# Performance work log

Hardware: AMD Instinct MI355X
Metric: run time of the kernel (lower is better)

## Reference

```python
import jax, jax.numpy as jnp
import numpy as np

WINDOW_SIZE = 128
LOOK_BACKWARD = 1
LOOK_FORWARD = 0  # causal
PAD_VALUE = -1


def look_around(x, backward=LOOK_BACKWARD, forward=LOOK_FORWARD, pad_value=PAD_VALUE):
    # x: [..., windows, window_size, ...]; pad along the windows axis (axis=1)
    # and concatenate shifted copies along the window_size axis (axis=2).
    w = x.shape[1]
    pad_width = [(0, 0), (backward, forward)] + [(0, 0)] * (x.ndim - 2)
    padded = jnp.pad(x, pad_width, constant_values=pad_value)
    return jnp.concatenate([padded[:, i:i + w] for i in range(forward + backward + 1)], axis=2)


def setup_inputs() -> dict:
    key = jax.random.key(0)
    kq, kk, kv = jax.random.split(key, 3)
    shape = (2, 16, 8192, 64)
    return {
        "q": jax.random.normal(kq, shape, dtype=jnp.float32),
        "k": jax.random.normal(kk, shape, dtype=jnp.float32),
        "v": jax.random.normal(kv, shape, dtype=jnp.float32),
    }


def reference(q, k, v):
    shape = q.shape
    t, e = shape[-2], shape[-1]
    ws = WINDOW_SIZE
    assert t % ws == 0
    windows = t // ws
    scale = e ** (-0.5)

    # merge batch and head dims
    bq, bk, bv = (x.reshape(-1, windows, ws, e) for x in (q, k, v))
    b = bq.shape[0]

    # position ticker, bucketed: [1, windows, ws]
    b_t = jnp.arange(t, dtype=jnp.int32).reshape(1, windows, ws)

    bk = look_around(bk)                      # [b, windows, 2*ws, e]
    bv = look_around(bv)
    bq_t = b_t                                # [1, windows, ws]
    bq_k = look_around(b_t)                   # [1, windows, 2*ws]

    # scores: [b, windows, ws, 2*ws]
    dots = jnp.einsum('bwie,bwje->bwij', bq, bk) * scale
    mask_value = -jnp.finfo(dots.dtype).max

    # causal mask: query position must be >= key position
    causal_mask = bq_t[..., :, None] < bq_k[..., None, :]
    # padding mask from look_around fill
    pad_mask = (bq_k == PAD_VALUE)[:, :, None, :]
    dots = jnp.where(causal_mask | pad_mask, mask_value, dots)

    attn = jax.nn.softmax(dots, axis=-1)
    out = jnp.einsum('bwij,bwje->bwie', attn, bv)  # [b, windows, ws, e]
    return out.reshape(shape)
```

## Files before the change

### kernel.cpp

```cpp
#include <hip/hip_runtime.h>
#include <stdint.h>

typedef float f32x16 __attribute__((ext_vector_type(16)));
typedef short bf16x8 __attribute__((ext_vector_type(8)));
typedef uint32_t u32;

#define T_LEN 8192
#define E_DIM 64
#define WSZ   128
#define NWIN  64
#define NBH   32
#define SCALE 0.125f

union Frag { u32 w[4]; bf16x8 v; };

__device__ __forceinline__ u32 pkbf(float a, float b) {
    u32 r;
    asm("v_cvt_pk_bf16_f32 %0, %1, %2" : "=v"(r) : "v"(a), "v"(b));
    return r;
}

__device__ __forceinline__ u32 kaddr(u32 key, u32 bir) {
    return (key * 128u + bir) ^ ((key & 15u) << 4);
}

__device__ __forceinline__ void pv_half(const f32x16& a, int ksbase, int h, int ql,
                                        long krow0, const float* __restrict__ vg,
                                        f32x16& o0, f32x16& o1) {
    u32 W[8];
#pragma unroll
    for (int j = 0; j < 8; ++j) W[j] = pkbf(a[2 * j], a[2 * j + 1]);
#pragma unroll
    for (int hi = 0; hi < 2; ++hi) {
        const u32 w0 = W[4 * hi + 0], w1 = W[4 * hi + 1];
        const u32 w2 = W[4 * hi + 2], w3 = W[4 * hi + 3];
        const u32 y0 = (u32)__shfl_xor((int)w0, 32);
        const u32 y1 = (u32)__shfl_xor((int)w1, 32);
        const u32 y2 = (u32)__shfl_xor((int)w2, 32);
        const u32 y3 = (u32)__shfl_xor((int)w3, 32);
        Frag au;
        au.w[0] = h ? y2 : w0;
        au.w[1] = h ? y3 : w1;
        au.w[2] = h ? w2 : y0;
        au.w[3] = h ? w3 : y1;
        const int ks = ksbase + hi;
        const long vr = (krow0 + (long)(16 * ks + 8 * h)) * E_DIM + ql;
        float v0[8], v1[8];
#pragma unroll
        for (int j = 0; j < 8; ++j) {
            v0[j] = vg[vr + (long)j * E_DIM];
            v1[j] = vg[vr + (long)j * E_DIM + 32];
        }
        Frag b0, b1;
#pragma unroll
        for (int j = 0; j < 4; ++j) {
            b0.w[j] = pkbf(v0[2 * j], v0[2 * j + 1]);
            b1.w[j] = pkbf(v1[2 * j], v1[2 * j + 1]);
        }
        o0 = __builtin_amdgcn_mfma_f32_32x32x16_bf16(au.v, b0.v, o0, 0, 0, 0);
        o1 = __builtin_amdgcn_mfma_f32_32x32x16_bf16(au.v, b1.v, o1, 0, 0, 0);
    }
}

__global__ __launch_bounds__(256, 3)
void lattn_kernel(const float* __restrict__ qg, const float* __restrict__ kg,
                  const float* __restrict__ vg, float* __restrict__ outg) {
    __shared__ __align__(16) char lds[32768];

    const int tid  = threadIdx.x;
    const int lane = tid & 63;
    const int wid  = tid >> 6;
    const int h    = lane >> 5;
    const int ql   = lane & 31;

    const int bid = blockIdx.x;
    const int swz = ((bid & 7) << 8) | (bid >> 3);
    const int bh  = swz >> 6;
    const int w   = swz & 63;

    const size_t qrow0 = (size_t)bh * T_LEN + (size_t)w * WSZ;
    const long   krow0 = (long)bh * T_LEN + (long)(w - 1) * WSZ;

    Frag qf[4];
    {
        const float* qp = qg + (qrow0 + (size_t)(wid * 32 + ql)) * E_DIM;
#pragma unroll
        for (int ks = 0; ks < 4; ++ks) {
            float4 a = *(const float4*)(qp + ks * 16 + h * 8);
            float4 b = *(const float4*)(qp + ks * 16 + h * 8 + 4);
            qf[ks].w[0] = pkbf(a.x * SCALE, a.y * SCALE);
            qf[ks].w[1] = pkbf(a.z * SCALE, a.w * SCALE);
            qf[ks].w[2] = pkbf(b.x * SCALE, b.y * SCALE);
            qf[ks].w[3] = pkbf(b.z * SCALE, b.w * SCALE);
        }
    }

#pragma unroll
    for (int i = 0; i < 16; ++i) {
        const int f   = i * 256 + tid;
        const int row = f >> 4;
        const int c   = f & 15;
        if (w > 0 || row >= 128) {
            const float4 kv = *(const float4*)(kg + (size_t)(krow0 + row) * E_DIM + c * 4);
            *(uint2*)(lds + kaddr((u32)row, (u32)c * 8u)) =
                make_uint2(pkbf(kv.x, kv.y), pkbf(kv.z, kv.w));
        }
    }
    __syncthreads();

    const int qpos = wid * 32 + ql;
    f32x16 o0, o1;
#pragma unroll
    for (int r = 0; r < 16; ++r) { o0[r] = 0.f; o1[r] = 0.f; }
    float den = 0.f;

    const int qp0 = (w == 0) ? 2 : 0;
    for (int qp = qp0; qp < 4; ++qp) {
#pragma unroll
        for (int kf2 = 0; kf2 < 2; ++kf2) {
            f32x16 a;
#pragma unroll
            for (int r = 0; r < 16; ++r) a[r] = 0.f;
#pragma unroll
            for (int ks = 0; ks < 4; ++ks) {
                const bf16x8 kf = *(const bf16x8*)(lds +
                    kaddr((u32)(64 * qp + 32 * kf2 + ql), (u32)(32 * ks + 16 * h)));
                a = __builtin_amdgcn_mfma_f32_32x32x16_bf16(kf, qf[ks].v, a, 0, 0, 0);
            }
            const int kb = 64 * qp + 32 * kf2 + 4 * h - 128;
#pragma unroll
            for (int r = 0; r < 16; ++r) {
                const int kr = kb + (r & 3) + 8 * (r >> 2);
                float p = __expf(a[r]);
                p = (kr <= qpos) ? p : 0.f;
                a[r] = p;
                den += p;
            }
            pv_half(a, 4 * qp + 2 * kf2, h, ql, krow0, vg, o0, o1);
        }
    }

    den += __shfl_xor(den, 32);
    const float invd = 1.f / den;

    float* ob = outg + (qrow0 + (size_t)(wid * 32)) * E_DIM;
#pragma unroll
    for (int r = 0; r < 16; ++r) {
        const int rowq = (r & 3) + 8 * (r >> 2) + 4 * h;
        const float dn = __shfl(invd, rowq);
        ob[(size_t)rowq * E_DIM + ql]      = o0[r] * dn;
        ob[(size_t)rowq * E_DIM + 32 + ql] = o1[r] * dn;
    }
}

extern "C" void kernel_launch(void* const* d_in, const int* in_sizes, int n_in,
                              void* d_out, int out_size, void* d_ws, size_t ws_size,
                              hipStream_t stream) {
    const float* q = (const float*)d_in[0];
    const float* k = (const float*)d_in[1];
    const float* v = (const float*)d_in[2];
    float* out = (float*)d_out;
    lattn_kernel<<<dim3(NBH * NWIN), dim3(256), 0, stream>>>(q, k, v, out);
}
```

Baseline: 261.6 us.

## Stage V in LDS as bf16 per 128-key block instead of strided global loads

The kernel now processes the two 128-key blocks one at a time. Each block's K and V are cooperatively loaded, converted to bf16 and stored into swizzled LDS halves, where before V was read per lane with strided scalar global loads inside the PV step. The causal mask is evaluated only for the diagonal block, and the occupancy hint rises from 3 to 4 blocks per CU. The cost is an extra barrier pair per block, 16-bit LDS gathers for the V fragments, and possible register pressure under the tighter launch bound.

After: 463.0 us. 77.0% more time.

```diff
diff --git a/kernel.cpp b/kernel.cpp
--- a/kernel.cpp
+++ b/kernel.cpp
@@ -20,49 +20,11 @@
     return r;
 }
 
-__device__ __forceinline__ u32 kaddr(u32 key, u32 bir) {
+__device__ __forceinline__ u32 swz(u32 key, u32 bir) {
     return (key * 128u + bir) ^ ((key & 15u) << 4);
 }
 
-__device__ __forceinline__ void pv_half(const f32x16& a, int ksbase, int h, int ql,
-                                        long krow0, const float* __restrict__ vg,
-                                        f32x16& o0, f32x16& o1) {
-    u32 W[8];
-#pragma unroll
-    for (int j = 0; j < 8; ++j) W[j] = pkbf(a[2 * j], a[2 * j + 1]);
-#pragma unroll
-    for (int hi = 0; hi < 2; ++hi) {
-        const u32 w0 = W[4 * hi + 0], w1 = W[4 * hi + 1];
-        const u32 w2 = W[4 * hi + 2], w3 = W[4 * hi + 3];
-        const u32 y0 = (u32)__shfl_xor((int)w0, 32);
-        const u32 y1 = (u32)__shfl_xor((int)w1, 32);
-        const u32 y2 = (u32)__shfl_xor((int)w2, 32);
-        const u32 y3 = (u32)__shfl_xor((int)w3, 32);
-        Frag au;
-        au.w[0] = h ? y2 : w0;
-        au.w[1] = h ? y3 : w1;
-        au.w[2] = h ? w2 : y0;
-        au.w[3] = h ? w3 : y1;
-        const int ks = ksbase + hi;
-        const long vr = (krow0 + (long)(16 * ks + 8 * h)) * E_DIM + ql;
-        float v0[8], v1[8];
-#pragma unroll
-        for (int j = 0; j < 8; ++j) {
-            v0[j] = vg[vr + (long)j * E_DIM];
-            v1[j] = vg[vr + (long)j * E_DIM + 32];
-        }
-        Frag b0, b1;
-#pragma unroll
-        for (int j = 0; j < 4; ++j) {
-            b0.w[j] = pkbf(v0[2 * j], v0[2 * j + 1]);
-            b1.w[j] = pkbf(v1[2 * j], v1[2 * j + 1]);
-        }
-        o0 = __builtin_amdgcn_mfma_f32_32x32x16_bf16(au.v, b0.v, o0, 0, 0, 0);
-        o1 = __builtin_amdgcn_mfma_f32_32x32x16_bf16(au.v, b1.v, o1, 0, 0, 0);
-    }
-}
-
-__global__ __launch_bounds__(256, 3)
+__global__ __launch_bounds__(256, 4)
 void lattn_kernel(const float* __restrict__ qg, const float* __restrict__ kg,
                   const float* __restrict__ vg, float* __restrict__ outg) {
     __shared__ __align__(16) char lds[32768];
@@ -74,9 +36,9 @@
     const int ql   = lane & 31;
 
     const int bid = blockIdx.x;
-    const int swz = ((bid & 7) << 8) | (bid >> 3);
-    const int bh  = swz >> 6;
-    const int w   = swz & 63;
+    const int sw  = ((bid & 7) << 8) | (bid >> 3);
+    const int bh  = sw >> 6;
+    const int w   = sw & 63;
 
     const size_t qrow0 = (size_t)bh * T_LEN + (size_t)w * WSZ;
     const long   krow0 = (long)bh * T_LEN + (long)(w - 1) * WSZ;
@@ -86,57 +48,95 @@
         const float* qp = qg + (qrow0 + (size_t)(wid * 32 + ql)) * E_DIM;
 #pragma unroll
         for (int ks = 0; ks < 4; ++ks) {
-            float4 a = *(const float4*)(qp + ks * 16 + h * 8);
-            float4 b = *(const float4*)(qp + ks * 16 + h * 8 + 4);
-            qf[ks].w[0] = pkbf(a.x * SCALE, a.y * SCALE);
-            qf[ks].w[1] = pkbf(a.z * SCALE, a.w * SCALE);
-            qf[ks].w[2] = pkbf(b.x * SCALE, b.y * SCALE);
-            qf[ks].w[3] = pkbf(b.z * SCALE, b.w * SCALE);
+            float4 x = *(const float4*)(qp + ks * 16 + h * 8);
+            float4 y = *(const float4*)(qp + ks * 16 + h * 8 + 4);
+            qf[ks].w[0] = pkbf(x.x * SCALE, x.y * SCALE);
+            qf[ks].w[1] = pkbf(x.z * SCALE, x.w * SCALE);
+            qf[ks].w[2] = pkbf(y.x * SCALE, y.y * SCALE);
+            qf[ks].w[3] = pkbf(y.z * SCALE, y.w * SCALE);
         }
     }
 
-#pragma unroll
-    for (int i = 0; i < 16; ++i) {
-        const int f   = i * 256 + tid;
-        const int row = f >> 4;
-        const int c   = f & 15;
-        if (w > 0 || row >= 128) {
-            const float4 kv = *(const float4*)(kg + (size_t)(krow0 + row) * E_DIM + c * 4);
-            *(uint2*)(lds + kaddr((u32)row, (u32)c * 8u)) =
-                make_uint2(pkbf(kv.x, kv.y), pkbf(kv.z, kv.w));
-        }
-    }
-    __syncthreads();
-
-    const int qpos = wid * 32 + ql;
     f32x16 o0, o1;
 #pragma unroll
     for (int r = 0; r < 16; ++r) { o0[r] = 0.f; o1[r] = 0.f; }
     float den = 0.f;
+    const int qpos = wid * 32 + ql;
 
-    const int qp0 = (w == 0) ? 2 : 0;
-    for (int qp = qp0; qp < 4; ++qp) {
+    const int kb0 = (w == 0) ? 1 : 0;
+    for (int kb = kb0; kb < 2; ++kb) {
+        __syncthreads();
+        {
+            const long rb = krow0 + (long)kb * 128;
 #pragma unroll
-        for (int kf2 = 0; kf2 < 2; ++kf2) {
+            for (int i = 0; i < 8; ++i) {
+                const int f = i * 256 + tid;
+                const int row = f >> 4, c = f & 15;
+                const size_t off = (size_t)(rb + row) * E_DIM + 4 * c;
+                const float4 kv = *(const float4*)(kg + off);
+                const float4 vv = *(const float4*)(vg + off);
+                *(uint2*)(lds + swz((u32)row, 8u * c)) =
+                    make_uint2(pkbf(kv.x, kv.y), pkbf(kv.z, kv.w));
+                *(uint2*)(lds + 16384 + swz((u32)row, 8u * c)) =
+                    make_uint2(pkbf(vv.x, vv.y), pkbf(vv.z, vv.w));
+            }
+        }
+        __syncthreads();
+
+        const bool MASK = (kb == 1);
+#pragma unroll
+        for (int b = 0; b < 4; ++b) {
             f32x16 a;
 #pragma unroll
             for (int r = 0; r < 16; ++r) a[r] = 0.f;
 #pragma unroll
             for (int ks = 0; ks < 4; ++ks) {
-                const bf16x8 kf = *(const bf16x8*)(lds +
-                    kaddr((u32)(64 * qp + 32 * kf2 + ql), (u32)(32 * ks + 16 * h)));
+                const bf16x8 kf = *(const bf16x8*)(lds + swz((u32)(32 * b + ql),
+                                                             (u32)(32 * ks + 16 * h)));
                 a = __builtin_amdgcn_mfma_f32_32x32x16_bf16(kf, qf[ks].v, a, 0, 0, 0);
             }
-            const int kb = 64 * qp + 32 * kf2 + 4 * h - 128;
 #pragma unroll
             for (int r = 0; r < 16; ++r) {
-                const int kr = kb + (r & 3) + 8 * (r >> 2);
                 float p = __expf(a[r]);
-                p = (kr <= qpos) ? p : 0.f;
+                if (MASK) {
+                    const int kr = 32 * b + 4 * h + (r & 3) + 8 * (r >> 2);
+                    p = (kr <= qpos) ? p : 0.f;
+                }
                 a[r] = p;
                 den += p;
             }
-            pv_half(a, 4 * qp + 2 * kf2, h, ql, krow0, vg, o0, o1);
+            u32 W[8];
+#pragma unroll
+            for (int j = 0; j < 8; ++j) W[j] = pkbf(a[2 * j], a[2 * j + 1]);
+#pragma unroll
+            for (int hi = 0; hi < 2; ++hi) {
+                const u32 w0 = W[4 * hi + 0], w1 = W[4 * hi + 1];
+                const u32 w2 = W[4 * hi + 2], w3 = W[4 * hi + 3];
+                const u32 y0 = (u32)__shfl_xor((int)w0, 32);
+                const u32 y1 = (u32)__shfl_xor((int)w1, 32);
+                const u32 y2 = (u32)__shfl_xor((int)w2, 32);
+                const u32 y3 = (u32)__shfl_xor((int)w3, 32);
+                Frag au;
+                au.w[0] = h ? y2 : w0;
+                au.w[1] = h ? y3 : w1;
+                au.w[2] = h ? w2 : y0;
+                au.w[3] = h ? w3 : y1;
+                const int k0 = 32 * b + 16 * hi + 8 * h;
+                u32 t0[8], t1[8];
+#pragma unroll
+                for (int j = 0; j < 8; ++j) {
+                    t0[j] = *(const uint16_t*)(lds + 16384 + swz((u32)(k0 + j), 2u * ql));
+                    t1[j] = *(const uint16_t*)(lds + 16384 + swz((u32)(k0 + j), 2u * (ql + 32)));
+                }
+                Frag b0, b1;
+#pragma unroll
+                for (int j = 0; j < 4; ++j) {
+                    b0.w[j] = t0[2 * j] | (t0[2 * j + 1] << 16);
+                    b1.w[j] = t1[2 * j] | (t1[2 * j + 1] << 16);
+                }
+                o0 = __builtin_amdgcn_mfma_f32_32x32x16_bf16(au.v, b0.v, o0, 0, 0, 0);
+                o1 = __builtin_amdgcn_mfma_f32_32x32x16_bf16(au.v, b1.v, o1, 0, 0, 0);
+            }
         }
     }
 
```
